# Performance work log

Hardware: AMD Instinct MI355X
Metric: run time of the kernel (lower is better)

## Reference

```python
import jax, jax.numpy as jnp
import numpy as np

DILATIONS = (1, 6, 12, 24, 36)
EPS = 1e-5


def conv2d(x, w, dil, pad):
    # x: (N,C,H,W), w: (O,I,3,3) or (O,I,1,1)
    return jax.lax.conv_general_dilated(
        x, w, window_strides=(1, 1), padding=[(pad, pad), (pad, pad)],
        rhs_dilation=(dil, dil), dimension_numbers=('NCHW', 'OIHW', 'NCHW'))


def _bilinear_sample(img, ys, xs):
    # img: (C,H,W); ys, xs: (H,W,9) float sampling coords; zero padding outside.
    C, H, W = img.shape
    y0 = jnp.floor(ys)
    x0 = jnp.floor(xs)
    wy1 = ys - y0
    wx1 = xs - x0
    wy0 = 1.0 - wy1
    wx0 = 1.0 - wx1

    def gather(yi, xi, w):
        valid = (yi >= 0) & (yi < H) & (xi >= 0) & (xi < W)
        yc = jnp.clip(yi, 0, H - 1).astype(jnp.int32)
        xc = jnp.clip(xi, 0, W - 1).astype(jnp.int32)
        v = img[:, yc, xc]  # (C,H,W,9)
        return v * (w * valid)[None]

    return (gather(y0, x0, wy0 * wx0) + gather(y0, x0 + 1, wy0 * wx1)
            + gather(y0 + 1, x0, wy1 * wx0) + gather(y0 + 1, x0 + 1, wy1 * wx1))


def deform_unfold(x, offset, dil, pad):
    # x: (N,C,H,W), offset: (N,18,H,W) interleaved (dy,dx) per 3x3 tap.
    N, C, H, W = x.shape
    ky = jnp.repeat(jnp.arange(3), 3)  # (9,)
    kx = jnp.tile(jnp.arange(3), 3)
    base_y = (jnp.arange(H)[:, None, None] + (ky * dil - pad)).astype(x.dtype)  # (H,1,9)
    base_x = (jnp.arange(W)[None, :, None] + (kx * dil - pad)).astype(x.dtype)  # (1,W,9)
    dy = jnp.transpose(offset[:, 0::2], (0, 2, 3, 1))  # (N,H,W,9)
    dx = jnp.transpose(offset[:, 1::2], (0, 2, 3, 1))
    ys = base_y[None] + dy  # (N,H,W,9)
    xs = base_x[None] + dx
    return jax.vmap(_bilinear_sample)(x, ys, xs)  # (N,C,H,W,9)


def dynamic_head(x, cat_ws, scale_w, gamma, beta):
    N, C, H, W = x.shape
    outs = [x]
    for w, dil in zip(cat_ws, DILATIONS):
        fo = conv2d(x, w, dil, dil)           # (N,27,H,W); pad == dil keeps size
        filt = jax.nn.softmax(jnp.transpose(fo[:, :9], (0, 2, 3, 1)), axis=-1)  # (N,H,W,9)
        off = fo[:, -18:]                      # (N,18,H,W)
        samp = deform_unfold(x, off, dil, dil)  # (N,C,H,W,9)
        outs.append(jnp.einsum('nchwk,nhwk->nchw', samp, filt))
    cat = jnp.concatenate(outs, axis=1)        # (N,6C,H,W)
    y = conv2d(cat, scale_w, 1, 0)             # (N,C,H,W)
    mean = jnp.mean(y, axis=(0, 2, 3))
    var = jnp.var(y, axis=(0, 2, 3))
    y = (y - mean[None, :, None, None]) * jax.lax.rsqrt(var + EPS)[None, :, None, None]
    return y * gamma[None, :, None, None] + beta[None, :, None, None]


def setup_inputs() -> dict:
    key = jax.random.key(0)
    ks = jax.random.split(key, 8)
    C = 512
    x = jax.random.normal(ks[0], (2, C, 64, 64), dtype=jnp.float32)
    cat_ws = [0.02 * jax.random.normal(ks[1 + i], (27, C, 3, 3), dtype=jnp.float32) for i in range(5)]
    scale_w = 0.02 * jax.random.normal(ks[6], (C, 6 * C, 1, 1), dtype=jnp.float32)
    gamma = jnp.ones((C,), dtype=jnp.float32)
    beta = jnp.zeros((C,), dtype=jnp.float32)
    return {'x': x, 'w1': cat_ws[0], 'w2': cat_ws[1], 'w3': cat_ws[2],
            'w4': cat_ws[3], 'w5': cat_ws[4], 'scale_w': scale_w,
            'gamma': gamma, 'beta': beta}


def reference(x, w1, w2, w3, w4, w5, scale_w, gamma, beta):
    return dynamic_head(x, (w1, w2, w3, w4, w5), scale_w, gamma, beta)
```

## Files before the change

kernel.cpp:

```cpp
#include <hip/hip_runtime.h>

typedef short short8 __attribute__((ext_vector_type(8)));
typedef float f32x4 __attribute__((ext_vector_type(4)));

#define CST 3072

__device__ __forceinline__ float bf2f(short s) {
  unsigned u = ((unsigned)(unsigned short)s) << 16;
  return __builtin_bit_cast(float, u);
}
__device__ __forceinline__ short f2bf(float f) {
  unsigned u = __builtin_bit_cast(unsigned, f);
  u = (u + 0x7FFFu + ((u >> 16) & 1u)) >> 16;
  return (short)u;
}
__device__ __forceinline__ void gl16(const short* g, short* l) {
  __builtin_amdgcn_global_load_lds(
      (const __attribute__((address_space(1))) unsigned*)g,
      (__attribute__((address_space(3))) unsigned*)l, 16, 0, 0);
}

__global__ void k_prep(const float* __restrict__ sw,
                       const float* __restrict__ w1, const float* __restrict__ w2,
                       const float* __restrict__ w3, const float* __restrict__ w4,
                       const float* __restrict__ w5,
                       short* __restrict__ wbf, short* __restrict__ wdr,
                       float* __restrict__ stats) {
  int idx = blockIdx.x * 256 + threadIdx.x;
  const int NS = 512 * 3072;
  const int NW = 5 * 9 * 32 * 512;
  if (idx < NS) {
    wbf[idx] = f2bf(sw[idx]);
  } else if (idx < NS + NW) {
    int j = idx - NS;
    int c = j & 511;
    int t2 = j >> 9;
    int oc = t2 & 31;
    int t3 = t2 >> 5;
    int tap = t3 % 9;
    int di = t3 / 9;
    float v = 0.f;
    if (oc < 27) {
      const float* wp = (di == 0) ? w1 : (di == 1) ? w2 : (di == 2) ? w3 : (di == 3) ? w4 : w5;
      v = wp[((oc * 512 + c) * 3 + tap / 3) * 3 + tap % 3];
    }
    wdr[j] = f2bf(v);
  } else if (idx < NS + NW + 1024) {
    stats[idx - NS - NW] = 0.f;
  }
}

__global__ __launch_bounds__(256) void k_transx(const float* __restrict__ x,
                                                short* __restrict__ cat) {
  __shared__ float tile[64][65];
  int b = blockIdx.x;
  int cblk = b & 7, h = (b >> 3) & 63, n = b >> 9;
  int c0 = cblk * 64;
  int t = threadIdx.x;
  int lw = t & 63, grp = t >> 6;
  const float* xp = x + (((size_t)n * 512 + c0) * 64 + h) * 64;
#pragma unroll
  for (int i = 0; i < 16; ++i) {
    int cl = grp * 16 + i;
    tile[cl][lw] = xp[(size_t)cl * 4096 + lw];
  }
  __syncthreads();
  int cl = t & 63;
  size_t mbase = ((size_t)n * 64 + h) * 64;
#pragma unroll
  for (int i = 0; i < 16; ++i) {
    int w = grp * 16 + i;
    cat[(mbase + w) * CST + c0 + cl] = f2bf(tile[cl][w]);
  }
}

__global__ __launch_bounds__(256) void k_conv(const short* __restrict__ xsrc,
                                              const short* __restrict__ wdr_all,
                                              int* __restrict__ ctab) {
  __shared__ short Bs[16384];
  __shared__ float fo[4][16][33];
  int tid = threadIdx.x;
  int wave = tid >> 6, lane = tid & 63;
  int l15 = lane & 15, quad = lane >> 4;
  int b = blockIdx.x;
  int di = b >> 7;
  int loc = b & 127;
  const int DIL[5] = {1, 6, 12, 24, 36};
  int d = DIL[di];
  int tile4 = (loc & 7) * 16 + (loc >> 3);
  int h = tile4 & 63, n = tile4 >> 6;
  int tile = tile4 * 4 + wave;
  int m = tile * 16 + l15;
  int w = m & 63;
  f32x4 acc0 = {0.f, 0.f, 0.f, 0.f}, acc1 = {0.f, 0.f, 0.f, 0.f};
  const short8 z8 = {0, 0, 0, 0, 0, 0, 0, 0};
  int soff[8];
  short* sdst[8];
#pragma unroll
  for (int it = 0; it < 8; ++it) {
    int q = it * 256 + tid;
    soff[it] = ((q >> 2) & 31) * 512 + (q >> 7) * 32 + (q & 3) * 8;
    sdst[it] = Bs + q * 8;
  }
  const short* wbase = wdr_all + (size_t)di * 9 * 32 * 512;
#pragma unroll
  for (int t = 0; t < 9; ++t) {
    int ty = t / 3, tx = t % 3;
    int hh = h + (ty - 1) * d;
    if ((unsigned)hh < 64u) {
      __syncthreads();
      const short* src = wbase + t * 32 * 512;
#pragma unroll
      for (int it = 0; it < 8; ++it) gl16(src + soff[it], sdst[it]);
      int ww = w + (tx - 1) * d;
      bool ok = (unsigned)ww < 64u;
      int mrow = (n << 12) + (hh << 6) + (ok ? ww : w);
      const short* arow = xsrc + (size_t)mrow * CST + quad * 8;
      short8 a[16];
#pragma unroll
      for (int ks = 0; ks < 16; ++ks) {
        short8 av = *(const short8*)(arow + ks * 32);
        a[ks] = ok ? av : z8;
      }
      __syncthreads();
#pragma unroll
      for (int ks = 0; ks < 16; ++ks) {
        short8 b0 = *(const short8*)(Bs + ks * 1024 + l15 * 32 + quad * 8);
        short8 b1 = *(const short8*)(Bs + ks * 1024 + (l15 + 16) * 32 + quad * 8);
        acc0 = __builtin_amdgcn_mfma_f32_16x16x32_bf16(a[ks], b0, acc0, 0, 0, 0);
        acc1 = __builtin_amdgcn_mfma_f32_16x16x32_bf16(a[ks], b1, acc1, 0, 0, 0);
      }
    }
  }
#pragma unroll
  for (int r = 0; r < 4; ++r) {
    fo[wave][quad * 4 + r][l15] = acc0[r];
    fo[wave][quad * 4 + r][l15 + 16] = acc1[r];
  }
  __syncthreads();
  if (lane < 16) {
    int p = lane;
    float mx = fo[wave][p][0];
#pragma unroll
    for (int k = 1; k < 9; ++k) mx = fmaxf(mx, fo[wave][p][k]);
    float s = 0.f, e[9];
#pragma unroll
    for (int k = 0; k < 9; ++k) { e[k] = __expf(fo[wave][p][k] - mx); s += e[k]; }
    float inv = 1.f / s;
#pragma unroll
    for (int k = 0; k < 9; ++k) fo[wave][p][k] = e[k] * inv;
  }
  __syncthreads();
#pragma unroll
  for (int t3 = 0; t3 < 3; ++t3) {
    int task = t3 * 48 + lane;
    if (lane < 48) {
      int p = (task * 57) >> 9;
      int k = task - p * 9;
      float f = fo[wave][p][k];
      float dy = fo[wave][p][9 + 2 * k];
      float dx = fo[wave][p][10 + 2 * k];
      int mm = tile * 16 + p;
      int hh = (mm >> 6) & 63, ww = mm & 63;
      float ys = (float)(hh + (k / 3 - 1) * d) + dy;
      float xs = (float)(ww + (k % 3 - 1) * d) + dx;
      float y0f = floorf(ys), x0f = floorf(xs);
      float wy1 = ys - y0f, wx1 = xs - x0f;
      float wy0 = 1.f - wy1, wx0 = 1.f - wx1;
      int y0 = (int)y0f, x0 = (int)x0f;
      int4 ent;
      int* ep = (int*)&ent;
#pragma unroll
      for (int cy = 0; cy < 2; ++cy)
#pragma unroll
        for (int cx = 0; cx < 2; ++cx) {
          int yy = y0 + cy, xx = x0 + cx;
          bool v = ((unsigned)yy < 64u) && ((unsigned)xx < 64u);
          float wt = f * (cy ? wy1 : wy0) * (cx ? wx1 : wx0);
          int row = v ? (yy * 64 + xx) : 0;
          unsigned wb = v ? (unsigned)(unsigned short)f2bf(wt) : 0u;
          ep[cy * 2 + cx] = row | (int)(wb << 16);
        }
      ((int4*)ctab)[((size_t)di * 8192 + mm) * 9 + k] = ent;
    }
  }
}

__global__ __launch_bounds__(256, 4) void k_samp(const short* __restrict__ xsrc,
                                                 short* __restrict__ cat,
                                                 const int* __restrict__ ctab) {
  int tid = threadIdx.x;
  int wv = __builtin_amdgcn_readfirstlane(tid >> 6);
  int lane = tid & 63;
  int b = blockIdx.x;
  int di = b >> 11;
  int loc = b & 2047;
  int m = (loc & 7) * 1024 + (loc >> 3) * 4 + wv;
  int n = m >> 12;
  const int4* tp = (const int4*)ctab + ((size_t)di * 8192 + m) * 9;
  const short* xb = xsrc + (size_t)(n << 12) * CST + lane * 8;
  float acc[8] = {0.f, 0.f, 0.f, 0.f, 0.f, 0.f, 0.f, 0.f};
#pragma unroll
  for (int k = 0; k < 9; ++k) {
    int4 e = tp[k];
    const int* ep = (const int*)&e;
#pragma unroll
    for (int c = 0; c < 4; ++c) {
      int dw = ep[c];
      float wt = __builtin_bit_cast(float, (unsigned)dw & 0xFFFF0000u);
      int row = dw & 0xFFFF;
      const short8 vv = *(const short8*)(xb + (size_t)row * CST);
#pragma unroll
      for (int j = 0; j < 8; ++j) acc[j] += wt * bf2f(vv[j]);
    }
  }
  short8 o8;
#pragma unroll
  for (int j = 0; j < 8; ++j) o8[j] = f2bf(acc[j]);
  *(short8*)(cat + (size_t)m * CST + 512 * (di + 1) + lane * 8) = o8;
}

__global__ __launch_bounds__(256) void k_gemm(const short* __restrict__ A,
                                              const short* __restrict__ B,
                                              short* __restrict__ Y) {
  __shared__ short As[128 * 64];
  __shared__ short Bs[128 * 64];
  int tid = threadIdx.x;
  int wave = tid >> 6, lane = tid & 63;
  int l15 = lane & 15, quad = lane >> 4;
  int bid = blockIdx.x;
  int xcd = bid & 7, s = bid >> 3;
  int mt = xcd * 8 + (s >> 3);
  int nz = s & 7;
  int nt = nz & 3, kh = nz >> 2;
  int m0 = mt * 128, n0 = nt * 128;
  int kbeg = kh * 1536;
  int wm = (wave >> 1) * 64, wn = (wave & 1) * 64;
  f32x4 acc[4][4];
  f32x4 zz = {0.f, 0.f, 0.f, 0.f};
#pragma unroll
  for (int i = 0; i < 4; ++i)
#pragma unroll
    for (int j = 0; j < 4; ++j) acc[i][j] = zz;
  const short* agp[4];
  const short* bgp[4];
  short* adst[4];
  short* bdst[4];
#pragma unroll
  for (int it = 0; it < 4; ++it) {
    int q = it * 256 + tid;
    int row = q >> 3;
    int c8g = (q & 7) ^ (row & 7);
    agp[it] = A + (size_t)(m0 + row) * CST + kbeg + c8g * 8;
    bgp[it] = B + (size_t)(n0 + row) * CST + kbeg + c8g * 8;
    adst[it] = As + q * 8;
    bdst[it] = Bs + q * 8;
  }
  int slotbA = (wm + l15) & 7;
  int slotbB = (wn + l15) & 7;
#pragma unroll 1
  for (int ks = 0; ks < 24; ++ks) {
    int ko = ks * 64;
    __syncthreads();
#pragma unroll
    for (int it = 0; it < 4; ++it) gl16(agp[it] + ko, adst[it]);
#pragma unroll
    for (int it = 0; it < 4; ++it) gl16(bgp[it] + ko, bdst[it]);
    __syncthreads();
#pragma unroll
    for (int kk = 0; kk < 2; ++kk) {
      int sa = ((quad + kk * 4) ^ slotbA) * 8;
      int sb = ((quad + kk * 4) ^ slotbB) * 8;
      short8 af[4], bf[4];
#pragma unroll
      for (int i = 0; i < 4; ++i)
        af[i] = *(const short8*)(As + (wm + i * 16 + l15) * 64 + sa);
#pragma unroll
      for (int j = 0; j < 4; ++j)
        bf[j] = *(const short8*)(Bs + (wn + j * 16 + l15) * 64 + sb);
#pragma unroll
      for (int i = 0; i < 4; ++i)
#pragma unroll
        for (int j = 0; j < 4; ++j)
          acc[i][j] = __builtin_amdgcn_mfma_f32_16x16x32_bf16(af[i], bf[j], acc[i][j], 0, 0, 0);
    }
  }
  short* Yp = Y + (size_t)kh * (8192 * 512);
#pragma unroll
  for (int i = 0; i < 4; ++i) {
    int row = m0 + wm + i * 16 + quad * 4;
#pragma unroll
    for (int j = 0; j < 4; ++j) {
      int col = n0 + wn + j * 16 + l15;
#pragma unroll
      for (int r = 0; r < 4; ++r)
        Yp[(size_t)(row + r) * 512 + col] = f2bf(acc[i][j][r]);
    }
  }
}

__global__ __launch_bounds__(256) void k_stats(const short* __restrict__ Y,
                                               float* __restrict__ stats) {
  const short* Y1 = Y + (size_t)8192 * 512;
  int tid = threadIdx.x;
  int mb = blockIdx.x * 32;
  float s0 = 0.f, q0 = 0.f, s1 = 0.f, q1 = 0.f;
  for (int r = 0; r < 32; ++r) {
    size_t ro = (size_t)(mb + r) * 512;
    float v0 = bf2f(Y[ro + tid]) + bf2f(Y1[ro + tid]);
    float v1 = bf2f(Y[ro + tid + 256]) + bf2f(Y1[ro + tid + 256]);
    s0 += v0; q0 += v0 * v0;
    s1 += v1; q1 += v1 * v1;
  }
  atomicAdd(&stats[tid], s0);
  atomicAdd(&stats[tid + 256], s1);
  atomicAdd(&stats[512 + tid], q0);
  atomicAdd(&stats[512 + tid + 256], q1);
}

__global__ __launch_bounds__(256) void k_norm(const short* __restrict__ Y,
                                              const float* __restrict__ stats,
                                              const float* __restrict__ gamma,
                                              const float* __restrict__ beta,
                                              float* __restrict__ out) {
  __shared__ float tile[64][65];
  const short* Y1 = Y + (size_t)8192 * 512;
  int b = blockIdx.x;
  int cblk = b & 7, h = (b >> 3) & 63, n = b >> 9;
  int c0 = cblk * 64;
  int t = threadIdx.x;
  int cl = t & 63, grp = t >> 6;
  int c = c0 + cl;
  float mean = stats[c] * (1.f / 8192.f);
  float var = stats[512 + c] * (1.f / 8192.f) - mean * mean;
  float Ai = gamma[c] * rsqrtf(var + 1e-5f);
  float Bi = beta[c] - mean * Ai;
  size_t mbase = ((size_t)n * 64 + h) * 64;
#pragma unroll
  for (int i = 0; i < 16; ++i) {
    int w = grp * 16 + i;
    size_t ro = (mbase + w) * 512 + c;
    tile[w][cl] = (bf2f(Y[ro]) + bf2f(Y1[ro])) * Ai + Bi;
  }
  __syncthreads();
  float* op = out + (((size_t)n * 512 + c0) * 64 + h) * 64;
#pragma unroll
  for (int i = 0; i < 16; ++i) {
    int c2 = grp * 16 + i;
    op[(size_t)c2 * 4096 + cl] = tile[cl][c2];
  }
}

extern "C" void kernel_launch(void* const* d_in, const int* in_sizes, int n_in,
                              void* d_out, int out_size, void* d_ws, size_t ws_size,
                              hipStream_t stream) {
  const float* x  = (const float*)d_in[0];
  const float* w1 = (const float*)d_in[1];
  const float* w2 = (const float*)d_in[2];
  const float* w3 = (const float*)d_in[3];
  const float* w4 = (const float*)d_in[4];
  const float* w5 = (const float*)d_in[5];
  const float* sw = (const float*)d_in[6];
  const float* gamma = (const float*)d_in[7];
  const float* beta  = (const float*)d_in[8];
  float* out = (float*)d_out;

  char* ws = (char*)d_ws;
  short* cat   = (short*)ws;
  short* wbf   = (short*)(ws + 50331648);
  short* wdr   = (short*)(ws + 53477376);
  short* yb    = (short*)(ws + 54951936);
  float* stats = (float*)(ws + 71729152);
  int*   ctab  = (int*)(ws + 71733248);

  k_prep<<<9028, 256, 0, stream>>>(sw, w1, w2, w3, w4, w5, wbf, wdr, stats);
  k_transx<<<1024, 256, 0, stream>>>(x, cat);
  k_conv<<<640, 256, 0, stream>>>(cat, wdr, ctab);
  k_samp<<<10240, 256, 0, stream>>>(cat, cat, ctab);
  k_gemm<<<512, 256, 0, stream>>>(cat, wbf, yb);
  k_stats<<<256, 256, 0, stream>>>(yb, stats);
  k_norm<<<1024, 256, 0, stream>>>(yb, stats, gamma, beta, out);
}
```

Measured before the change: 239.9 us.

## Stage conv A rows through LDS with XOR-swizzled async loads

The offset/filter conv kernel now loads each wave's 16 input rows into a per-wave LDS buffer with global_load_lds, instead of holding 16 short8 registers per lane loaded directly from global memory. The B weight layout in LDS is changed to a row-major layout with an XOR swizzle on the lane index to avoid bank conflicts. This is meant to coalesce A loads, cut register pressure, and make the loads asynchronous. In exchange it adds 64KB of LDS per block, which can reduce occupancy.

```diff
diff --git a/kernel.cpp b/kernel.cpp
--- a/kernel.cpp
+++ b/kernel.cpp
@@ -77,6 +77,7 @@
 __global__ __launch_bounds__(256) void k_conv(const short* __restrict__ xsrc,
                                               const short* __restrict__ wdr_all,
                                               int* __restrict__ ctab) {
+  __shared__ short As[4][8192];
   __shared__ short Bs[16384];
   __shared__ float fo[4][16][33];
   int tid = threadIdx.x;
@@ -90,45 +91,45 @@
   int tile4 = (loc & 7) * 16 + (loc >> 3);
   int h = tile4 & 63, n = tile4 >> 6;
   int tile = tile4 * 4 + wave;
-  int m = tile * 16 + l15;
-  int w = m & 63;
   f32x4 acc0 = {0.f, 0.f, 0.f, 0.f}, acc1 = {0.f, 0.f, 0.f, 0.f};
   const short8 z8 = {0, 0, 0, 0, 0, 0, 0, 0};
-  int soff[8];
-  short* sdst[8];
-#pragma unroll
-  for (int it = 0; it < 8; ++it) {
-    int q = it * 256 + tid;
-    soff[it] = ((q >> 2) & 31) * 512 + (q >> 7) * 32 + (q & 3) * 8;
-    sdst[it] = Bs + q * 8;
-  }
+  short* aw = As[wave];
+  int lx[8];
+#pragma unroll
+  for (int r = 0; r < 8; ++r) lx[r] = (lane ^ r) * 8;
   const short* wbase = wdr_all + (size_t)di * 9 * 32 * 512;
+  int rowb = (n << 12);
 #pragma unroll
   for (int t = 0; t < 9; ++t) {
     int ty = t / 3, tx = t % 3;
     int hh = h + (ty - 1) * d;
     if ((unsigned)hh < 64u) {
       __syncthreads();
-      const short* src = wbase + t * 32 * 512;
-#pragma unroll
-      for (int it = 0; it < 8; ++it) gl16(src + soff[it], sdst[it]);
-      int ww = w + (tx - 1) * d;
-      bool ok = (unsigned)ww < 64u;
-      int mrow = (n << 12) + (hh << 6) + (ok ? ww : w);
-      const short* arow = xsrc + (size_t)mrow * CST + quad * 8;
-      short8 a[16];
-#pragma unroll
-      for (int ks = 0; ks < 16; ++ks) {
-        short8 av = *(const short8*)(arow + ks * 32);
-        a[ks] = ok ? av : z8;
+      const short* bsrc = wbase + t * 32 * 512;
+#pragma unroll
+      for (int j = 0; j < 8; ++j) {
+        int oc = wave * 8 + j;
+        gl16(bsrc + oc * 512 + lx[j], Bs + oc * 512);
+      }
+      int ww0 = wave * 16 + (tx - 1) * d;
+      int rb = rowb + (hh << 6);
+#pragma unroll
+      for (int r = 0; r < 16; ++r) {
+        int wwr = ww0 + r;
+        int wwc = wwr < 0 ? 0 : (wwr > 63 ? 63 : wwr);
+        gl16(xsrc + (size_t)(rb + wwc) * CST + lx[r & 7], aw + r * 512);
       }
       __syncthreads();
+      bool okv = (unsigned)(ww0 + l15) < 64u;
 #pragma unroll
       for (int ks = 0; ks < 16; ++ks) {
-        short8 b0 = *(const short8*)(Bs + ks * 1024 + l15 * 32 + quad * 8);
-        short8 b1 = *(const short8*)(Bs + ks * 1024 + (l15 + 16) * 32 + quad * 8);
-        acc0 = __builtin_amdgcn_mfma_f32_16x16x32_bf16(a[ks], b0, acc0, 0, 0, 0);
-        acc1 = __builtin_amdgcn_mfma_f32_16x16x32_bf16(a[ks], b1, acc1, 0, 0, 0);
+        int ch = (((ks * 4 + quad) ^ (l15 & 7))) * 8;
+        short8 a = *(const short8*)(aw + l15 * 512 + ch);
+        if (!okv) a = z8;
+        short8 b0 = *(const short8*)(Bs + l15 * 512 + ch);
+        short8 b1 = *(const short8*)(Bs + (l15 + 16) * 512 + ch);
+        acc0 = __builtin_amdgcn_mfma_f32_16x16x32_bf16(a, b0, acc0, 0, 0, 0);
+        acc1 = __builtin_amdgcn_mfma_f32_16x16x32_bf16(a, b1, acc1, 0, 0, 0);
       }
     }
   }
```

Result: no change. 237.4 us (-1.0%).
